# Optimization experiments

Measured on AMD Instinct MI355X. Metric: run time of the kernel, lower is better.

The kernel has to match this reference:

```python
import jax, jax.numpy as jnp
import numpy as np

NUM_ENT = 14541
NUM_REL = 474
D = 400
B = 32
N_CAND = 14505


def setup_inputs() -> dict:
    key = jax.random.key(0)
    k0, k1, k2, k4, k5 = jax.random.split(key, 5)
    return {
        "arg0_1": jax.random.normal(k0, (NUM_ENT, D), dtype=jnp.float32),   # entity embeddings
        "arg1_1": jax.random.normal(k1, (NUM_REL, D), dtype=jnp.float32),   # relation centers
        "arg2_1": jax.random.uniform(k2, (NUM_REL, D), dtype=jnp.float32),  # relation offsets (box widths)
        "arg3_1": jnp.ones((1,), dtype=jnp.float32),                        # margin gamma
        "arg4_1": jax.random.randint(k4, (B, 2), 0, NUM_REL),               # (head_id, rel_id) pairs
        "arg5_1": jax.random.randint(k5, (4, N_CAND), 0, NUM_ENT),          # candidate entity ids (row 0 used)
    }


def reference(arg0_1, arg1_1, arg2_1, arg3_1, arg4_1, arg5_1):
    # Gather heads / relation params
    head = arg0_1[arg4_1[:, 0]]            # [B, D]
    rel_c = arg1_1[arg4_1[:, 1]]           # [B, D]
    rel_o = arg2_1[arg4_1[:, 1]]           # [B, D]

    query = (head + rel_c)[:, None, :]     # [B, 1, D] box center
    offset = rel_o[:, None, :]             # [B, 1, D] box width

    # Candidate tail embeddings: only row 0 of arg5_1 is used in the graph
    cand = arg0_1[arg5_1[0].reshape(-1)][None, :, :]  # [1, N_CAND, D]

    d = jnp.abs(cand - query)                           # [B, N_CAND, D]
    dist_outside = jax.nn.relu(d - offset).sum(-1)      # [B, N_CAND]
    dist_inside = jnp.abs(jnp.minimum(d, offset)).sum(-1)

    return arg3_1 - dist_outside - 0.02 * dist_inside   # [B, N_CAND]
```

## Files before the change

### kernel.cpp

```cpp
#include <hip/hip_runtime.h>

#define DIM     400
#define B       32
#define NCAND   14505
#define NROUND  3627
#define TSTRIPS 256
#define THREADS 256

__global__ __launch_bounds__(THREADS, 2)
void score_kernel(const float* __restrict__ ent,
                  const float* __restrict__ relc,
                  const float* __restrict__ relo,
                  const float* __restrict__ onev,
                  const int*   __restrict__ pairs,
                  const int*   __restrict__ cidx,
                  float* __restrict__ out) {
    const int fid  = blockIdx.x;
    const int xcd  = fid & 7;
    const int rest = fid >> 3;
    const int bq   = rest & 7;
    const int tc   = rest >> 3;
    const int t    = xcd + 8 * tc;

    const int tid  = threadIdx.x;
    const int lane = tid & 63;
    const int u    = lane & 15;
    const int g    = lane >> 4;
    const int b    = __builtin_amdgcn_readfirstlane(bq * 4 + (tid >> 6));

    const int hd = pairs[b * 2 + 0];
    const int rl = pairs[b * 2 + 1];
    const float4* hb = (const float4*)(ent  + (size_t)hd * DIM) + u;
    const float4* cb = (const float4*)(relc + (size_t)rl * DIM) + u;
    const float4* ob = (const float4*)(relo + (size_t)rl * DIM) + u;

    float4 q[7], o[7];
    float oa = 0.f;
#pragma unroll
    for (int k = 0; k < 6; ++k) {
        float4 h = hb[16 * k], c = cb[16 * k];
        q[k] = make_float4(h.x + c.x, h.y + c.y, h.z + c.z, h.w + c.w);
        o[k] = ob[16 * k];
        oa += o[k].x + o[k].y + o[k].z + o[k].w;
    }
    if (u < 4) {
        float4 h = hb[96], c = cb[96];
        q[6] = make_float4(h.x + c.x, h.y + c.y, h.z + c.z, h.w + c.w);
        o[6] = ob[96];
        oa += o[6].x + o[6].y + o[6].z + o[6].w;
    }
    oa += __shfl_xor(oa, 1);
    oa += __shfl_xor(oa, 2);
    oa += __shfl_xor(oa, 4);
    oa += __shfl_xor(oa, 8);
    const float base = onev[0] + 0.98f * oa;

    const float4* entu = (const float4*)ent + u;

    for (int rr = t; rr < NROUND; rr += TSTRIPS) {
        const int cand = 4 * rr + g;
        const int ci   = cidx[cand < NCAND ? cand : NCAND - 1];
        const float4* p = entu + (size_t)ci * 100;

        float4 cbuf[7];
#pragma unroll
        for (int k = 0; k < 6; ++k) cbuf[k] = p[16 * k];
        if (u < 4) cbuf[6] = p[96];

        float am0 = 0.f, ad0 = 0.f, am1 = 0.f, ad1 = 0.f;
#define E(vc, vq, vo, AM, AD)                     \
        {                                         \
            float d_ = (vc) - (vq);               \
            AM += fmaxf(fabsf(d_), (vo));         \
            AD += fabsf(d_);                      \
        }
#define F4(k, AM, AD)                             \
        E(cbuf[k].x, q[k].x, o[k].x, AM, AD)      \
        E(cbuf[k].y, q[k].y, o[k].y, AM, AD)      \
        E(cbuf[k].z, q[k].z, o[k].z, AM, AD)      \
        E(cbuf[k].w, q[k].w, o[k].w, AM, AD)

        F4(0, am0, ad0) F4(1, am1, ad1)
        F4(2, am0, ad0) F4(3, am1, ad1)
        F4(4, am0, ad0) F4(5, am1, ad1)
        if (u < 4) { F4(6, am0, ad0) }
#undef F4
#undef E

        float s_ = fmaf(-0.98f, am0 + am1, -0.02f * (ad0 + ad1));
        s_ += __shfl_xor(s_, 1);
        s_ += __shfl_xor(s_, 2);
        s_ += __shfl_xor(s_, 4);
        s_ += __shfl_xor(s_, 8);

        if (u == 0 && cand < NCAND)
            out[(size_t)b * NCAND + cand] = base + s_;
    }
}

extern "C" void kernel_launch(void* const* d_in, const int* in_sizes, int n_in,
                              void* d_out, int out_size, void* d_ws, size_t ws_size,
                              hipStream_t stream) {
    const float* ent   = (const float*)d_in[0];
    const float* relc  = (const float*)d_in[1];
    const float* relo  = (const float*)d_in[2];
    const float* onev  = (const float*)d_in[3];
    const int*   pairs = (const int*)d_in[4];
    const int*   cidx  = (const int*)d_in[5];
    float*       out   = (float*)d_out;

    const int grid = 8 * 8 * 32;
    score_kernel<<<grid, THREADS, 0, stream>>>(ent, relc, relo, onev, pairs, cidx, out);
}
```

Baseline: 46.16 us.

## Score all entities into workspace table then gather candidates via scatter kernel

Replaces the per-candidate gather-and-score kernel with a two-kernel scheme. The first kernel scores every entity sequentially for all 32 queries into a workspace table, reading the entity matrix contiguously. The second kernel looks up each candidate's score by index and adds the base term. This removes random gathered row reads at the cost of a second launch, scoring entities that are not candidates, and using strided scalar loads (25 floats per lane) instead of float4. The old kernel is kept as a fallback when the workspace is too small.

```diff
diff --git a/kernel.cpp b/kernel.cpp
--- a/kernel.cpp
+++ b/kernel.cpp
@@ -1,20 +1,103 @@
 #include <hip/hip_runtime.h>
 
 #define DIM     400
+#define NENT    14541
 #define B       32
 #define NCAND   14505
-#define NROUND  3627
-#define TSTRIPS 256
 #define THREADS 256
+#define NTILE   1818
+#define NSC     1814
+
+__global__ __launch_bounds__(512, 2)
+void score_ent(const float* __restrict__ ent,
+               const float* __restrict__ relc,
+               const float* __restrict__ relo,
+               const int*   __restrict__ pairs,
+               float* __restrict__ stab) {
+    const int tile = blockIdx.x;
+    const int e0   = tile * 8;
+    const int tid  = threadIdx.x;
+    const int wid  = tid >> 6;
+    const int lane = tid & 63;
+    const int u    = lane & 15;
+    const int g    = lane >> 4;
+    const int b    = 4 * wid + g;
+
+    const int hd = pairs[2 * b + 0];
+    const int rl = pairs[2 * b + 1];
+    const float* hp = ent  + (size_t)hd * DIM + 25 * u;
+    const float* cp = relc + (size_t)rl * DIM + 25 * u;
+    const float* op = relo + (size_t)rl * DIM + 25 * u;
+
+    float q[25], o[25];
+#pragma unroll
+    for (int k = 0; k < 25; ++k) {
+        q[k] = hp[k] + cp[k];
+        o[k] = op[k];
+    }
+
+    const int emax = (NENT - e0 < 8) ? (NENT - e0) : 8;
+    for (int c = 0; c < emax; ++c) {
+        const float* cr = ent + (size_t)(e0 + c) * DIM + 25 * u;
+        float am = 0.f, ad = 0.f;
+#pragma unroll
+        for (int k = 0; k < 25; ++k) {
+            float d = cr[k] - q[k];
+            float a = fabsf(d);
+            am += fmaxf(a, o[k]);
+            ad += a;
+        }
+        float s = fmaf(0.98f, am, 0.02f * ad);
+        s += __shfl_xor(s, 1);
+        s += __shfl_xor(s, 2);
+        s += __shfl_xor(s, 4);
+        s += __shfl_xor(s, 8);
+        if (u == 0)
+            stab[(size_t)b * NENT + e0 + c] = s;
+    }
+}
+
+__global__ __launch_bounds__(THREADS)
+void scatter_k(const float* __restrict__ stab,
+               const float* __restrict__ relo,
+               const float* __restrict__ onev,
+               const int*   __restrict__ pairs,
+               const int*   __restrict__ cidx,
+               float* __restrict__ out) {
+    const int blk = blockIdx.x;
+    const int b   = blk >> 3;
+    const int ch  = blk & 7;
+    const int tid = threadIdx.x;
+
+    const int rl = pairs[2 * b + 1];
+    float so = 0.f;
+    if (tid < 100) {
+        float4 v = ((const float4*)(relo + (size_t)rl * DIM))[tid];
+        so = v.x + v.y + v.z + v.w;
+    }
+    for (int off = 32; off; off >>= 1) so += __shfl_down(so, off);
+    __shared__ float red[4];
+    if ((tid & 63) == 0) red[tid >> 6] = so;
+    __syncthreads();
+    const float base = onev[0] + 0.98f * (red[0] + red[1] + red[2] + red[3]);
+
+    const float* sb = stab + (size_t)b * NENT;
+    const int n0 = ch * NSC;
+    const int n1 = (n0 + NSC < NCAND) ? n0 + NSC : NCAND;
+    for (int n = n0 + tid; n < n1; n += THREADS) {
+        const int ci = cidx[n];
+        out[(size_t)b * NCAND + n] = base - sb[ci];
+    }
+}
 
 __global__ __launch_bounds__(THREADS, 2)
-void score_kernel(const float* __restrict__ ent,
-                  const float* __restrict__ relc,
-                  const float* __restrict__ relo,
-                  const float* __restrict__ onev,
-                  const int*   __restrict__ pairs,
-                  const int*   __restrict__ cidx,
-                  float* __restrict__ out) {
+void score_f32(const float* __restrict__ ent,
+               const float* __restrict__ relc,
+               const float* __restrict__ relo,
+               const float* __restrict__ onev,
+               const int*   __restrict__ pairs,
+               const int*   __restrict__ cidx,
+               float* __restrict__ out) {
     const int fid  = blockIdx.x;
     const int xcd  = fid & 7;
     const int rest = fid >> 3;
@@ -57,17 +140,6 @@
 
     const float4* entu = (const float4*)ent + u;
 
-    for (int rr = t; rr < NROUND; rr += TSTRIPS) {
-        const int cand = 4 * rr + g;
-        const int ci   = cidx[cand < NCAND ? cand : NCAND - 1];
-        const float4* p = entu + (size_t)ci * 100;
-
-        float4 cbuf[7];
-#pragma unroll
-        for (int k = 0; k < 6; ++k) cbuf[k] = p[16 * k];
-        if (u < 4) cbuf[6] = p[96];
-
-        float am0 = 0.f, ad0 = 0.f, am1 = 0.f, ad1 = 0.f;
 #define E(vc, vq, vo, AM, AD)                     \
         {                                         \
             float d_ = (vc) - (vq);               \
@@ -80,12 +152,21 @@
         E(cbuf[k].z, q[k].z, o[k].z, AM, AD)      \
         E(cbuf[k].w, q[k].w, o[k].w, AM, AD)
 
+    for (int rr = t; rr < 3627; rr += 256) {
+        const int cand = 4 * rr + g;
+        const int ci   = cidx[cand < NCAND ? cand : NCAND - 1];
+        const float4* p = entu + (size_t)ci * 100;
+
+        float4 cbuf[7];
+#pragma unroll
+        for (int k = 0; k < 6; ++k) cbuf[k] = p[16 * k];
+        if (u < 4) cbuf[6] = p[96];
+
+        float am0 = 0.f, ad0 = 0.f, am1 = 0.f, ad1 = 0.f;
         F4(0, am0, ad0) F4(1, am1, ad1)
         F4(2, am0, ad0) F4(3, am1, ad1)
         F4(4, am0, ad0) F4(5, am1, ad1)
         if (u < 4) { F4(6, am0, ad0) }
-#undef F4
-#undef E
 
         float s_ = fmaf(-0.98f, am0 + am1, -0.02f * (ad0 + ad1));
         s_ += __shfl_xor(s_, 1);
@@ -96,6 +177,8 @@
         if (u == 0 && cand < NCAND)
             out[(size_t)b * NCAND + cand] = base + s_;
     }
+#undef F4
+#undef E
 }
 
 extern "C" void kernel_launch(void* const* d_in, const int* in_sizes, int n_in,
@@ -109,6 +192,14 @@
     const int*   cidx  = (const int*)d_in[5];
     float*       out   = (float*)d_out;
 
-    const int grid = 8 * 8 * 32;
-    score_kernel<<<grid, THREADS, 0, stream>>>(ent, relc, relo, onev, pairs, cidx, out);
-}
+    const size_t need = (size_t)B * NENT * sizeof(float);
+
+    if (ws_size >= need) {
+        float* stab = (float*)d_ws;
+        score_ent<<<NTILE, 512, 0, stream>>>(ent, relc, relo, pairs, stab);
+        scatter_k<<<B * 8, THREADS, 0, stream>>>(stab, relo, onev, pairs, cidx, out);
+    } else {
+        score_f32<<<8 * 8 * 32, THREADS, 0, stream>>>(
+            ent, relc, relo, onev, pairs, cidx, out);
+    }
+}
```

New measurement: 69.12 us. 49.7% more time.
